# Performance work log

Measured on AMD Instinct MI355X. Metric: run time of the kernel, lower is better.

## Reference

```python
import jax, jax.numpy as jnp
import numpy as np

N = 50000      # nodes
E = 800000     # edges (before self-loops)
DIN, H1, H2, OUT = 128, 128, 64, 40
LN_EPS = 1e-5


def setup_inputs() -> dict:
    key = jax.random.key(0)
    ks = jax.random.split(key, 16)
    s = lambda d: 1.0 / np.sqrt(d)
    inp = {
        "x": jax.random.normal(ks[0], (N, DIN), jnp.float32),
        "edge_index": jax.random.randint(ks[1], (2, E), 0, N, dtype=jnp.int64),
        # GCNConv weights (applied as x @ W) and biases
        "W1": jax.random.normal(ks[2], (DIN, H1), jnp.float32) * s(DIN),
        "b1": jnp.zeros((H1,), jnp.float32),
        "W2": jax.random.normal(ks[3], (H1, H2), jnp.float32) * s(H1),
        "b2": jnp.zeros((H2,), jnp.float32),
        "W3": jax.random.normal(ks[4], (H2, H2), jnp.float32) * s(H2),
        "b3": jnp.zeros((H2,), jnp.float32),
        # LayerNorms
        "g1": jnp.ones((H1,), jnp.float32),
        "be1": jnp.zeros((H1,), jnp.float32),
        "g2": jnp.ones((H2,), jnp.float32),
        "be2": jnp.zeros((H2,), jnp.float32),
        # post_mp MLP head
        "Wp1": jax.random.normal(ks[5], (H2, H2), jnp.float32) * s(H2),
        "bp1": jnp.zeros((H2,), jnp.float32),
        "Wp2": jax.random.normal(ks[6], (H2, OUT), jnp.float32) * s(H2),
        "bp2": jnp.zeros((OUT,), jnp.float32),
    }
    return inp


def _layer_norm(x, g, b):
    mu = jnp.mean(x, axis=-1, keepdims=True)
    var = jnp.mean((x - mu) ** 2, axis=-1, keepdims=True)
    return (x - mu) * jax.lax.rsqrt(var + LN_EPS) * g + b


def _gcn(x, src, dst, norm, W, b):
    # PyG GCNConv: linear first, then normalized gather/scatter-add, bias last
    h = x @ W                                  # [N, H]
    msg = h[src] * norm[:, None]               # [E+N, H] gather
    out = jax.ops.segment_sum(msg, dst, num_segments=N)  # scatter-add
    return out + b


def reference(x, edge_index, W1, b1, W2, b2, W3, b3, g1, be1, g2, be2,
              Wp1, bp1, Wp2, bp2):
    loops = jnp.arange(N, dtype=edge_index.dtype)
    src = jnp.concatenate([edge_index[0], loops])  # add self-loops
    dst = jnp.concatenate([edge_index[1], loops])
    # symmetric normalization D^{-1/2} (A+I) D^{-1/2} (same graph all layers)
    deg = jax.ops.segment_sum(jnp.ones_like(src, dtype=x.dtype), dst,
                              num_segments=N)
    dinv = jnp.where(deg > 0, jax.lax.rsqrt(jnp.maximum(deg, 1.0)), 0.0)
    norm = dinv[src] * dinv[dst]

    h = _gcn(x, src, dst, norm, W1, b1)
    h = _layer_norm(jax.nn.relu(h), g1, be1)
    h = _gcn(h, src, dst, norm, W2, b2)
    h = _layer_norm(jax.nn.relu(h), g2, be2)
    emb = _gcn(h, src, dst, norm, W3, b3)      # emb = conv output, pre-ReLU
    h = jax.nn.relu(emb)
    h = (h @ Wp1 + bp1) @ Wp2 + bp2            # post_mp: two stacked Linears
    return emb, jax.nn.log_softmax(h, axis=1)
```

## Files before the change

### kernel.cpp

```cpp
#include <hip/hip_runtime.h>
#include <hip/hip_bf16.h>

#define DIN 128
#define HID1 128
#define HID2 64
#define OUTD 40
#define NCHUNK 128

typedef __attribute__((ext_vector_type(8))) short bf16x8;
typedef __attribute__((ext_vector_type(4))) float f32x4;

__device__ __forceinline__ float bf2f(unsigned int u) {
    union { unsigned int i; float f; } c;
    c.i = u << 16;
    return c.f;
}
__device__ __forceinline__ unsigned short f2bf(float f) {
    union { float f; unsigned int i; } c; c.f = f;
    unsigned int r = c.i + 0x7FFFu + ((c.i >> 16) & 1u);
    return (unsigned short)(r >> 16);
}
__device__ __forceinline__ unsigned int packbf(float lo, float hi) {
    return (unsigned int)f2bf(lo) | ((unsigned int)f2bf(hi) << 16);
}

__device__ __forceinline__ int get_src(const int* ei, int E, int e, int e64) {
    return e64 ? ei[2 * e] : ei[e];
}
__device__ __forceinline__ int get_dst(const int* ei, int E, int e, int e64) {
    return e64 ? ei[2 * (E + e)] : ei[E + e];
}

struct WCvt {
    const void* p[14];
    int sz[14];
    int off[14];
    int tobf[14];
    int cols[14];
};

__launch_bounds__(1024)
__global__ void posA_kernel(const unsigned short* __restrict__ xu,
                            const int* __restrict__ ei,
                            int* __restrict__ flags,
                            int* __restrict__ pos,
                            unsigned int* __restrict__ hist,
                            int E, int N) {
    __shared__ unsigned int h32[25000];
    __shared__ int sh2[2];
    const int NW = (N + 1) >> 1;
    const int b = blockIdx.x;
    const int t = threadIdx.x;
    if (b < NCHUNK) {
        if (t == 0) sh2[0] = 0;
        for (int w = t; w < NW; w += 1024) h32[w] = 0u;
        __syncthreads();
        int zodd = 0;
        for (int k = t; k < 1024; k += 1024)
            if (ei[2 * k + 1] == 0) zodd++;
        if (zodd) atomicAdd(&sh2[0], zodd);
        __syncthreads();
        const int e64 = (sh2[0] > 512) ? 1 : 0;
        const int CH = (E + NCHUNK - 1) / NCHUNK;
        const int lo = b * CH;
        int hi = lo + CH; if (hi > E) hi = E;
        for (int e = lo + t; e < hi; e += 1024) {
            int d = e64 ? ei[2 * (E + e)] : ei[E + e];
            if ((unsigned)d < (unsigned)N) {
                unsigned sh = (unsigned)(d & 1) << 4;
                unsigned old = atomicAdd(&h32[d >> 1], 1u << sh);
                pos[e] = (int)((old >> sh) & 0xffffu);
            } else {
                pos[e] = -1;
            }
        }
        __syncthreads();
        unsigned int* hb = hist + (size_t)b * NW;
        for (int w = t; w < NW; w += 1024) hb[w] = h32[w];
    } else {
        if (t < 2) sh2[t] = 0;
        __syncthreads();
        int bad = 0;
        for (int k = t; k < 2048; k += 1024) {
            float v = bf2f(xu[2 * k]);
            float a = fabsf(v);
            if (!(a <= 1e4f) || (v != 0.f && a < 1e-4f)) bad++;
        }
        int zodd = 0;
        for (int k = t; k < 1024; k += 1024)
            if (ei[2 * k + 1] == 0) zodd++;
        if (bad) atomicAdd(&sh2[0], bad);
        if (zodd) atomicAdd(&sh2[1], zodd);
        __syncthreads();
        if (t == 0) {
            flags[0] = (sh2[0] > 512) ? 1 : 0;
            flags[1] = (sh2[1] > 512) ? 1 : 0;
        }
    }
}

__launch_bounds__(256)
__global__ void phaseB_kernel(const unsigned int* __restrict__ hist,
                              unsigned int* __restrict__ basev,
                              int* __restrict__ cnt, int* __restrict__ bsum,
                              int N, int PB,
                              WCvt wc, unsigned short* __restrict__ wbf,
                              float* __restrict__ wf,
                              const int* __restrict__ flags) {
    __shared__ int red[256];
    const int NW = (N + 1) >> 1;
    int t = threadIdx.x;
    int blk = blockIdx.x;
    if (blk < PB) {
        int w = blk * 256 + t;
        unsigned run0 = 0, run1 = 0;
        if (w < NW) {
            #pragma unroll 4
            for (int b = 0; b < NCHUNK; ++b) {
                unsigned u = hist[(size_t)b * NW + w];
                basev[(size_t)b * NW + w] = (run0 & 0xffffu) | (run1 << 16);
                run0 += u & 0xffffu;
                run1 += u >> 16;
            }
            cnt[2 * w] = (int)run0;
            if (2 * w + 1 < N) cnt[2 * w + 1] = (int)run1;
        }
        int tot = 0;
        if (w < NW) tot = (int)run0 + ((2 * w + 1 < N) ? (int)run1 : 0);
        red[t] = tot;
        __syncthreads();
        #pragma unroll
        for (int off = 64; off >= 1; off >>= 1) {
            if ((t & 127) < off) red[t] += red[t + off];
            __syncthreads();
        }
        if (t == 0) bsum[2 * blk] = red[0];
        if (t == 128) bsum[2 * blk + 1] = red[128];
    } else {
        int xf32 = flags[0];
        int stride = (gridDim.x - PB) * 256;
        int tid = (blk - PB) * 256 + t;
        for (int a = 0; a < 14; ++a) {
            const float* pf = (const float*)wc.p[a];
            const unsigned short* pb = (const unsigned short*)wc.p[a];
            int n = wc.sz[a], off = wc.off[a], tobf = wc.tobf[a];
            int cols = wc.cols[a];
            int rows = tobf ? (n / cols) : 0;
            for (int i = tid; i < n; i += stride) {
                float v = xf32 ? pf[i] : bf2f(pb[i]);
                if (tobf) {
                    int k = i / cols, m = i % cols;
                    wbf[off + m * rows + k] = f2bf(v);
                } else {
                    wf[off + i] = v;
                }
            }
        }
    }
}

__global__ void scatter_kernel(const int* __restrict__ ei, const int* __restrict__ indptr,
                               const int* __restrict__ pos, const float* __restrict__ dinv,
                               const unsigned int* __restrict__ basev,
                               int2* __restrict__ csr_sn,
                               int E, int N, const int* __restrict__ flags) {
    int e64 = flags[1];
    int CH = (E + NCHUNK - 1) / NCHUNK;
    int NW = (N + 1) >> 1;
    int base = (blockIdx.x * blockDim.x + threadIdx.x) * 4;
    #pragma unroll
    for (int u = 0; u < 4; ++u) {
        int e = base + u;
        if (e < E) {
            int p = pos[e];
            if (p >= 0) {
                int bb = e / CH;
                int d = get_dst(ei, E, e, e64);
                int s = get_src(ei, E, e, e64);
                if ((unsigned)s >= (unsigned)N) s = 0;
                float nrm = dinv[s] * dinv[d];
                unsigned bw = basev[(size_t)bb * NW + (d >> 1)];
                int bval = (d & 1) ? (int)(bw >> 16) : (int)(bw & 0xffffu);
                int slot = indptr[d] + bval + p;
                csr_sn[slot] = make_int2(s, __float_as_int(nrm));
            }
        }
    }
}


template<typename AT>
__device__ __forceinline__ bf16x8 ld_afrag(const AT* p);
template<>
__device__ __forceinline__ bf16x8 ld_afrag<unsigned short>(const unsigned short* p) {
    return *(const bf16x8*)p;
}
template<>
__device__ __forceinline__ bf16x8 ld_afrag<float>(const float* p) {
    float4 a = *(const float4*)p;
    float4 b = *(const float4*)(p + 4);
    bf16x8 r;
    r[0] = (short)f2bf(a.x); r[1] = (short)f2bf(a.y);
    r[2] = (short)f2bf(a.z); r[3] = (short)f2bf(a.w);
    r[4] = (short)f2bf(b.x); r[5] = (short)f2bf(b.y);
    r[6] = (short)f2bf(b.z); r[7] = (short)f2bf(b.w);
    return r;
}

template<int K, int M, typename AT>
__device__ __forceinline__ void mm_body(const AT* __restrict__ A,
                                        const unsigned short* __restrict__ WT,
                                        unsigned short* __restrict__ C, int N,
                                        unsigned short (*Ws)[K + 8], int bx) {
    int tid = threadIdx.x;
    for (int idx = tid; idx < M * K / 8; idx += 256) {
        int r = idx / (K / 8), c8 = idx % (K / 8);
        *(uint4*)&Ws[r][c8 * 8] = *(const uint4*)&WT[r * K + c8 * 8];
    }
    __syncthreads();
    int w = tid >> 6, lane = tid & 63;
    int m = lane & 15, q = lane >> 4;
    int row_a = bx * 64 + w * 16 + m;
    if (row_a >= N) row_a = N - 1;
    const AT* arow = A + (size_t)row_a * K;
    f32x4 acc[M / 16];
    #pragma unroll
    for (int t = 0; t < M / 16; ++t) acc[t] = (f32x4){0.f, 0.f, 0.f, 0.f};
    #pragma unroll
    for (int ks = 0; ks < K / 32; ++ks) {
        int k0 = ks * 32 + q * 8;
        bf16x8 a = ld_afrag<AT>(arow + k0);
        #pragma unroll
        for (int t = 0; t < M / 16; ++t) {
            bf16x8 b = *(const bf16x8*)&Ws[t * 16 + m][k0];
            acc[t] = __builtin_amdgcn_mfma_f32_16x16x32_bf16(a, b, acc[t], 0, 0, 0);
        }
    }
    int rbase = bx * 64 + w * 16 + q * 4;
    #pragma unroll
    for (int reg = 0; reg < 4; ++reg) {
        int row = rbase + reg;
        if (row < N) {
            #pragma unroll
            for (int t = 0; t < M / 16; ++t)
                C[(size_t)row * M + t * 16 + m] = f2bf(acc[t][reg]);
        }
    }
}

template<int K, int M>
__launch_bounds__(256)
__global__ void emit_mm_kernel(const int* __restrict__ cnt, const int* __restrict__ bsum,
                               int* __restrict__ indptr, float* __restrict__ dinv,
                               int N, int NB,
                               const void* __restrict__ A,
                               const unsigned short* __restrict__ WT,
                               unsigned short* __restrict__ C,
                               const int* __restrict__ flags) {
    __shared__ unsigned short Ws[M][K + 8];
    int blk = blockIdx.x;
    int t = threadIdx.x;
    if (blk < NB) {
        int* part = (int*)&Ws[0][0];
        int* sh   = part + 256;
        part[t] = (t < NB) ? bsum[t] : 0;
        __syncthreads();
        for (int off = 1; off < 256; off <<= 1) {
            int v = (t >= off) ? part[t - off] : 0;
            __syncthreads();
            part[t] += v;
            __syncthreads();
        }
        int bbase = (blk > 0) ? part[blk - 1] : 0;
        int total = part[255];
        int i = blk * 256 + t;
        int c = (i < N) ? cnt[i] : 0;
        sh[t] = c;
        __syncthreads();
        for (int off = 1; off < 256; off <<= 1) {
            int v = (t >= off) ? sh[t - off] : 0;
            __syncthreads();
            sh[t] += v;
            __syncthreads();
        }
        if (i < N) {
            int excl = sh[t] - c + bbase;
            indptr[i] = excl;
            dinv[i] = 1.0f / sqrtf((float)(c + 1));
        }
        if (blk == NB - 1 && t == 0) indptr[N] = total;
    } else {
        int bx = blk - NB;
        if (flags[0]) mm_body<K, M, float>((const float*)A, WT, C, N, Ws, bx);
        else          mm_body<K, M, unsigned short>((const unsigned short*)A, WT, C, N, Ws, bx);
    }
}

template<int K, int M>
__launch_bounds__(256)
__global__ void mm_bf_kernel(const unsigned short* __restrict__ A,
                             const unsigned short* __restrict__ WT,
                             unsigned short* __restrict__ C, int N) {
    __shared__ unsigned short Ws[M][K + 8];
    mm_body<K, M, unsigned short>(A, WT, C, N, Ws, blockIdx.x);
}


template<int VPL>
__device__ __forceinline__ void gacc1(float* acc, const unsigned short* r, float n) {
    if constexpr (VPL == 8) {
        uint4 u = *(const uint4*)r;
        acc[0] += bf2f(u.x & 0xffffu) * n; acc[1] += bf2f(u.x >> 16) * n;
        acc[2] += bf2f(u.y & 0xffffu) * n; acc[3] += bf2f(u.y >> 16) * n;
        acc[4] += bf2f(u.z & 0xffffu) * n; acc[5] += bf2f(u.z >> 16) * n;
        acc[6] += bf2f(u.w & 0xffffu) * n; acc[7] += bf2f(u.w >> 16) * n;
    } else {
        uint2 u = *(const uint2*)r;
        acc[0] += bf2f(u.x & 0xffffu) * n; acc[1] += bf2f(u.x >> 16) * n;
        acc[2] += bf2f(u.y & 0xffffu) * n; acc[3] += bf2f(u.y >> 16) * n;
    }
}

template<int VPL>
__device__ __forceinline__ void gacc8(float* acc,
                                      const unsigned short* const* rp,
                                      const float* nv) {
    if constexpr (VPL == 8) {
        uint4 u[8];
        #pragma unroll
        for (int i = 0; i < 8; ++i) u[i] = *(const uint4*)rp[i];
        #pragma unroll
        for (int i = 0; i < 8; ++i) {
            float n = nv[i];
            acc[0] += bf2f(u[i].x & 0xffffu) * n; acc[1] += bf2f(u[i].x >> 16) * n;
            acc[2] += bf2f(u[i].y & 0xffffu) * n; acc[3] += bf2f(u[i].y >> 16) * n;
            acc[4] += bf2f(u[i].z & 0xffffu) * n; acc[5] += bf2f(u[i].z >> 16) * n;
            acc[6] += bf2f(u[i].w & 0xffffu) * n; acc[7] += bf2f(u[i].w >> 16) * n;
        }
    } else {
        uint2 u[8];
        #pragma unroll
        for (int i = 0; i < 8; ++i) u[i] = *(const uint2*)rp[i];
        #pragma unroll
        for (int i = 0; i < 8; ++i) {
            float n = nv[i];
            acc[0] += bf2f(u[i].x & 0xffffu) * n; acc[1] += bf2f(u[i].x >> 16) * n;
            acc[2] += bf2f(u[i].y & 0xffffu) * n; acc[3] += bf2f(u[i].y >> 16) * n;
        }
    }
}

template<int H, bool RELU_LN, bool EMB>
__launch_bounds__(256)
__global__ void agg_kernel(const unsigned short* __restrict__ h,
                           const int* __restrict__ indptr,
                           const int2* __restrict__ csr_sn,
                           const float* __restrict__ dinv,
                           const float* __restrict__ bias,
                           const float* __restrict__ gamma,
                           const float* __restrict__ beta,
                           unsigned short* __restrict__ out,
                           void* __restrict__ out_emb,
                           int N, const int* __restrict__ flags) {
    constexpr int VPL = H / 16;
    __shared__ int2 lsn[4][4][32];
    int w = threadIdx.x >> 6;
    int lane = threadIdx.x & 63;
    int g = lane >> 4;
    int idx = lane & 15;
    int node = blockIdx.x * 16 + w * 4 + g;
    bool active = node < N;
    int nd = active ? node : N - 1;
    float di = dinv[nd];
    int c0 = idx * VPL;
    float acc[VPL];
    #pragma unroll
    for (int v = 0; v < VPL; ++v) acc[v] = 0.f;
    gacc1<VPL>(acc, h + (size_t)nd * H + c0, di * di);
    int beg = indptr[nd], end = indptr[nd + 1];
    for (int base = beg; base < end; base += 32) {
        int m = end - base; if (m > 32) m = 32;
        lsn[w][g][idx]      = (idx < m)      ? csr_sn[base + idx]      : make_int2(0, 0);
        lsn[w][g][idx + 16] = (idx + 16 < m) ? csr_sn[base + idx + 16] : make_int2(0, 0);
        int rounds = (m + 7) >> 3;
        int j = 0;
        for (int rr = 0; rr < rounds; ++rr, j += 8) {
            const unsigned short* rp[8];
            float nv[8];
            #pragma unroll
            for (int i = 0; i < 8; ++i) {
                int2 e = lsn[w][g][j + i];
                rp[i] = h + (size_t)e.x * H + c0;
                nv[i] = __int_as_float(e.y);
            }
            gacc8<VPL>(acc, rp, nv);
        }
    }
    #pragma unroll
    for (int v = 0; v < VPL; ++v) acc[v] += bias[c0 + v];
    if constexpr (RELU_LN) {
        #pragma unroll
        for (int v = 0; v < VPL; ++v) acc[v] = fmaxf(acc[v], 0.f);
        float s = 0.f, sq = 0.f;
        #pragma unroll
        for (int v = 0; v < VPL; ++v) { s += acc[v]; sq += acc[v] * acc[v]; }
        #pragma unroll
        for (int off = 8; off >= 1; off >>= 1) {
            s += __shfl_xor(s, off, 64);
            sq += __shfl_xor(sq, off, 64);
        }
        float mu = s * (1.0f / H);
        float var = fmaxf(sq * (1.0f / H) - mu * mu, 0.f);
        float inv = 1.0f / sqrtf(var + 1e-5f);
        #pragma unroll
        for (int v = 0; v < VPL; ++v)
            acc[v] = (acc[v] - mu) * inv * gamma[c0 + v] + beta[c0 + v];
    }
    if (active) {
        unsigned short* orow = out + (size_t)node * H + c0;
        if constexpr (VPL == 8) {
            uint4 p;
            p.x = packbf(acc[0], acc[1]); p.y = packbf(acc[2], acc[3]);
            p.z = packbf(acc[4], acc[5]); p.w = packbf(acc[6], acc[7]);
            *(uint4*)orow = p;
        } else {
            uint2 p; p.x = packbf(acc[0], acc[1]); p.y = packbf(acc[2], acc[3]);
            *(uint2*)orow = p;
        }
        if constexpr (EMB) {
            if (flags[0]) {
                float* o = (float*)out_emb + (size_t)node * H + c0;
                #pragma unroll
                for (int v4 = 0; v4 < VPL / 4; ++v4)
                    *(float4*)(o + v4 * 4) = make_float4(acc[v4 * 4], acc[v4 * 4 + 1],
                                                         acc[v4 * 4 + 2], acc[v4 * 4 + 3]);
            } else {
                unsigned short* o = (unsigned short*)out_emb + (size_t)node * H + c0;
                #pragma unroll
                for (int v2 = 0; v2 < VPL / 2; ++v2)
                    ((unsigned int*)o)[v2] = packbf(acc[v2 * 2], acc[v2 * 2 + 1]);
            }
        }
    }
}


__launch_bounds__(256)
__global__ void head_kernel(const unsigned short* __restrict__ emb,
                            const float* __restrict__ Wp1,
                            const float* __restrict__ bp1,
                            const float* __restrict__ Wp2,
                            const float* __restrict__ bp2,
                            void* __restrict__ d_out, int N,
                            const int* __restrict__ flags) {
    __shared__ float Est[64][68];
    __shared__ float W1s[64][64];
    __shared__ float Tst[64][68];
    __shared__ float W2s[64][OUTD];
    __shared__ float b1s[64];
    __shared__ float b2s[OUTD];
    int tid = threadIdx.x;
    int row0 = blockIdx.x * 64;
    for (int i = tid; i < 64 * 64; i += 256) W1s[i >> 6][i & 63] = Wp1[i];
    for (int i = tid; i < 64 * OUTD; i += 256) W2s[i / OUTD][i % OUTD] = Wp2[i];
    if (tid < 64) b1s[tid] = bp1[tid];
    if (tid < OUTD) b2s[tid] = bp2[tid];
    for (int i = tid; i < 64 * 32; i += 256) {
        int r = i >> 5, kk = i & 31;
        int row = row0 + r;
        unsigned int u = (row < N) ? *(const unsigned int*)&emb[(size_t)row * 64 + kk * 2] : 0u;
        Est[kk * 2][r]     = fmaxf(bf2f(u & 0xffffu), 0.f);
        Est[kk * 2 + 1][r] = fmaxf(bf2f(u >> 16), 0.f);
    }
    __syncthreads();
    {
        int rg = tid >> 4, cg = tid & 15;
        int r = rg * 4, c = cg * 4;
        float acc[4][4];
        #pragma unroll
        for (int i = 0; i < 4; ++i)
            #pragma unroll
            for (int jj = 0; jj < 4; ++jj) acc[i][jj] = b1s[c + jj];
        #pragma unroll 4
        for (int k = 0; k < 64; ++k) {
            float4 a = *(const float4*)&Est[k][r];
            float4 wv = *(const float4*)&W1s[k][c];
            acc[0][0] += a.x * wv.x; acc[0][1] += a.x * wv.y; acc[0][2] += a.x * wv.z; acc[0][3] += a.x * wv.w;
            acc[1][0] += a.y * wv.x; acc[1][1] += a.y * wv.y; acc[1][2] += a.y * wv.z; acc[1][3] += a.y * wv.w;
            acc[2][0] += a.z * wv.x; acc[2][1] += a.z * wv.y; acc[2][2] += a.z * wv.z; acc[2][3] += a.z * wv.w;
            acc[3][0] += a.w * wv.x; acc[3][1] += a.w * wv.y; acc[3][2] += a.w * wv.z; acc[3][3] += a.w * wv.w;
        }
        #pragma unroll
        for (int i = 0; i < 4; ++i)
            #pragma unroll
            for (int jj = 0; jj < 4; ++jj) Tst[c + jj][r + i] = acc[i][jj];
    }
    __syncthreads();
    int row = tid >> 2, tc = tid & 3, o0 = tc * 10;
    int node = row0 + row;
    float u[10];
    #pragma unroll
    for (int o = 0; o < 10; ++o) u[o] = b2s[o0 + o];
    for (int c2 = 0; c2 < 64; ++c2) {
        float tv = Tst[c2][row];
        const float2* wp = (const float2*)&W2s[c2][o0];
        #pragma unroll
        for (int o2 = 0; o2 < 5; ++o2) {
            float2 wv = wp[o2];
            u[o2 * 2]     += tv * wv.x;
            u[o2 * 2 + 1] += tv * wv.y;
        }
    }
    float mx = u[0];
    #pragma unroll
    for (int o = 1; o < 10; ++o) mx = fmaxf(mx, u[o]);
    mx = fmaxf(mx, __shfl_xor(mx, 1, 64));
    mx = fmaxf(mx, __shfl_xor(mx, 2, 64));
    float sum = 0.f;
    #pragma unroll
    for (int o = 0; o < 10; ++o) sum += __expf(u[o] - mx);
    sum += __shfl_xor(sum, 1, 64);
    sum += __shfl_xor(sum, 2, 64);
    float lse = mx + __logf(sum);
    if (node < N) {
        if (flags[0]) {
            float* base = (float*)d_out + (size_t)N * HID2;
            float* op = base + (size_t)node * OUTD + o0;
            #pragma unroll
            for (int o = 0; o < 10; ++o) op[o] = u[o] - lse;
        } else {
            unsigned short* base = (unsigned short*)d_out + (size_t)N * HID2;
            unsigned int* op = (unsigned int*)(base + (size_t)node * OUTD + o0);
            #pragma unroll
            for (int o2 = 0; o2 < 5; ++o2)
                op[o2] = packbf(u[o2 * 2] - lse, u[o2 * 2 + 1] - lse);
        }
    }
}


extern "C" void kernel_launch(void* const* d_in, const int* in_sizes, int n_in,
                              void* d_out, int out_size, void* d_ws, size_t ws_size,
                              hipStream_t stream) {
    const unsigned short* xu = (const unsigned short*)d_in[0];
    const int*            ei = (const int*)d_in[1];

    const int N = in_sizes[0] / DIN;
    const int E = in_sizes[1] / 2;
    const int NW = (N + 1) / 2;

    size_t off = 0;
    auto take = [&](size_t bytes) {
        size_t cur = off;
        off += (bytes + 255) & ~(size_t)255;
        return cur;
    };
    char* ws = (char*)d_ws;
    int*   flags   = (int*)  (ws + take(256));
    int*   cnt     = (int*)  (ws + take((size_t)N * 4));
    float* dinv    = (float*)(ws + take((size_t)N * 4));
    int*   indptr  = (int*)  (ws + take((size_t)(N + 1) * 4));
    int*   pos     = (int*)  (ws + take((size_t)E * 4));
    int2*  csr_sn  = (int2*) (ws + take((size_t)E * 8));
    int*   bsum    = (int*)  (ws + take(((size_t)N / 256 + 4) * 4));
    unsigned int* hist  = (unsigned int*)(ws + take((size_t)NCHUNK * NW * 4));
    unsigned int* basev = (unsigned int*)(ws + take((size_t)NCHUNK * NW * 4));
    unsigned short* wbf = (unsigned short*)(ws + take(32768 * 2));
    float*          wf  = (float*)         (ws + take(8192 * 4));
    unsigned short* hbuf = (unsigned short*)(ws + take((size_t)N * DIN * 2));
    unsigned short* abuf = (unsigned short*)(ws + take((size_t)N * DIN * 2));
    (void)ws_size; (void)n_in; (void)out_size;

    const int TB = 256;
    dim3 blk(TB);
    const int NB = (N + 255) / 256;
    const int PB = (NW + 255) / 256;
    const int MMG = (N + 63) / 64;

    WCvt wc;
    int bfoff = 0, foff = 0;
    int offs[14];
    const int wcols[14] = {HID1, 0, HID2, 0, HID2, 0, 0, 0, 0, 0, 0, 0, 0, 0};
    for (int a = 0; a < 14; ++a) {
        int idx = a + 2;
        wc.p[a] = d_in[idx];
        wc.sz[a] = in_sizes[idx];
        int tobf = (idx == 2 || idx == 4 || idx == 6) ? 1 : 0;
        wc.tobf[a] = tobf;
        wc.cols[a] = tobf ? wcols[a] : 1;
        if (tobf) { wc.off[a] = bfoff; bfoff += in_sizes[idx]; }
        else      { wc.off[a] = foff;  foff  += in_sizes[idx]; }
        offs[a] = wc.off[a];
    }

    unsigned short* W1t = wbf + offs[0];
    unsigned short* W2t = wbf + offs[2];
    unsigned short* W3t = wbf + offs[4];
    float* b1f  = wf + offs[1];
    float* b2f  = wf + offs[3];
    float* b3f  = wf + offs[5];
    float* g1f  = wf + offs[6];
    float* be1f = wf + offs[7];
    float* g2f  = wf + offs[8];
    float* be2f = wf + offs[9];
    float* Wp1f = wf + offs[10];
    float* bp1f = wf + offs[11];
    float* Wp2f = wf + offs[12];
    float* bp2f = wf + offs[13];

    posA_kernel<<<dim3(NCHUNK + 1), dim3(1024), 0, stream>>>(
        xu, ei, flags, pos, hist, E, N);
    phaseB_kernel<<<dim3(PB + 64), blk, 0, stream>>>(
        hist, basev, cnt, bsum, N, PB, wc, wbf, wf, flags);
    emit_mm_kernel<DIN, HID1><<<dim3(NB + MMG), blk, 0, stream>>>(
        cnt, bsum, indptr, dinv, N, NB, d_in[0], W1t, hbuf, flags);
    scatter_kernel<<<dim3((E + 1023) / 1024), blk, 0, stream>>>(
        ei, indptr, pos, dinv, basev, csr_sn, E, N, flags);

    const int AGG = (N + 15) / 16;

    agg_kernel<HID1, true, false><<<dim3(AGG), blk, 0, stream>>>(
        hbuf, indptr, csr_sn, dinv, b1f, g1f, be1f, abuf, nullptr, N, flags);

    mm_bf_kernel<HID1, HID2><<<dim3(MMG), blk, 0, stream>>>(abuf, W2t, hbuf, N);
    agg_kernel<HID2, true, false><<<dim3(AGG), blk, 0, stream>>>(
        hbuf, indptr, csr_sn, dinv, b2f, g2f, be2f, abuf, nullptr, N, flags);

    mm_bf_kernel<HID2, HID2><<<dim3(MMG), blk, 0, stream>>>(abuf, W3t, hbuf, N);
    agg_kernel<HID2, false, true><<<dim3(AGG), blk, 0, stream>>>(
        hbuf, indptr, csr_sn, dinv, b3f, nullptr, nullptr, abuf, d_out, N, flags);

    head_kernel<<<dim3((N + 63) / 64), blk, 0, stream>>>(
        abuf, Wp1f, bp1f, Wp2f, bp2f, d_out, N, flags);
}
```

Before: 275.7 us.

## Fuse GCN aggregation with following matmul and head into combined kernels

Merges each aggregation+ReLU+LayerNorm step with the next layer's MFMA matmul, so normalized rows stay in shared memory instead of round-tripping through global memory. The final aggregation is fused with the post-MP MLP head and log-softmax. This removes three launches and several full-size intermediate writes and reads. In exchange each block does four nodes per wave-group sequentially before the matmul, which lowers the number of blocks and the latency hiding available to the gather loop.

```diff
diff --git a/kernel.cpp b/kernel.cpp
--- a/kernel.cpp
+++ b/kernel.cpp
@@ -296,15 +296,6 @@
     }
 }
 
-template<int K, int M>
-__launch_bounds__(256)
-__global__ void mm_bf_kernel(const unsigned short* __restrict__ A,
-                             const unsigned short* __restrict__ WT,
-                             unsigned short* __restrict__ C, int N) {
-    __shared__ unsigned short Ws[M][K + 8];
-    mm_body<K, M, unsigned short>(A, WT, C, N, Ws, blockIdx.x);
-}
-
 
 template<int VPL>
 __device__ __forceinline__ void gacc1(float* acc, const unsigned short* r, float n) {
@@ -350,38 +341,21 @@
     }
 }
 
-template<int H, bool RELU_LN, bool EMB>
-__launch_bounds__(256)
-__global__ void agg_kernel(const unsigned short* __restrict__ h,
-                           const int* __restrict__ indptr,
-                           const int2* __restrict__ csr_sn,
-                           const float* __restrict__ dinv,
-                           const float* __restrict__ bias,
-                           const float* __restrict__ gamma,
-                           const float* __restrict__ beta,
-                           unsigned short* __restrict__ out,
-                           void* __restrict__ out_emb,
-                           int N, const int* __restrict__ flags) {
-    constexpr int VPL = H / 16;
-    __shared__ int2 lsn[4][4][32];
-    int w = threadIdx.x >> 6;
-    int lane = threadIdx.x & 63;
-    int g = lane >> 4;
-    int idx = lane & 15;
-    int node = blockIdx.x * 16 + w * 4 + g;
-    bool active = node < N;
-    int nd = active ? node : N - 1;
-    float di = dinv[nd];
-    int c0 = idx * VPL;
-    float acc[VPL];
+template<int VPL, int H>
+__device__ __forceinline__ void agg_node(float* acc,
+                                         const unsigned short* __restrict__ h,
+                                         const int* __restrict__ indptr,
+                                         const int2* __restrict__ csr_sn,
+                                         int nd, float di, int c0,
+                                         int2 (*lsn), int idx) {
     #pragma unroll
     for (int v = 0; v < VPL; ++v) acc[v] = 0.f;
     gacc1<VPL>(acc, h + (size_t)nd * H + c0, di * di);
     int beg = indptr[nd], end = indptr[nd + 1];
     for (int base = beg; base < end; base += 32) {
         int m = end - base; if (m > 32) m = 32;
-        lsn[w][g][idx]      = (idx < m)      ? csr_sn[base + idx]      : make_int2(0, 0);
-        lsn[w][g][idx + 16] = (idx + 16 < m) ? csr_sn[base + idx + 16] : make_int2(0, 0);
+        lsn[idx]      = (idx < m)      ? csr_sn[base + idx]      : make_int2(0, 0);
+        lsn[idx + 16] = (idx + 16 < m) ? csr_sn[base + idx + 16] : make_int2(0, 0);
         int rounds = (m + 7) >> 3;
         int j = 0;
         for (int rr = 0; rr < rounds; ++rr, j += 8) {
@@ -389,18 +363,51 @@
             float nv[8];
             #pragma unroll
             for (int i = 0; i < 8; ++i) {
-                int2 e = lsn[w][g][j + i];
+                int2 e = lsn[j + i];
                 rp[i] = h + (size_t)e.x * H + c0;
                 nv[i] = __int_as_float(e.y);
             }
             gacc8<VPL>(acc, rp, nv);
         }
     }
-    #pragma unroll
-    for (int v = 0; v < VPL; ++v) acc[v] += bias[c0 + v];
-    if constexpr (RELU_LN) {
-        #pragma unroll
-        for (int v = 0; v < VPL; ++v) acc[v] = fmaxf(acc[v], 0.f);
+}
+
+
+template<int H, int M>
+__launch_bounds__(256)
+__global__ void aggmm_kernel(const unsigned short* __restrict__ h,
+                             const int* __restrict__ indptr,
+                             const int2* __restrict__ csr_sn,
+                             const float* __restrict__ dinv,
+                             const float* __restrict__ bias,
+                             const float* __restrict__ gamma,
+                             const float* __restrict__ beta,
+                             const unsigned short* __restrict__ WT,
+                             unsigned short* __restrict__ C, int N) {
+    constexpr int VPL = H / 16;
+    __shared__ unsigned short At[64][H + 8];
+    __shared__ unsigned short Ws[M][H + 8];
+    __shared__ int2 lsn[4][4][32];
+    int tid = threadIdx.x;
+    for (int i2 = tid; i2 < M * H / 8; i2 += 256) {
+        int r = i2 / (H / 8), c8 = i2 % (H / 8);
+        *(uint4*)&Ws[r][c8 * 8] = *(const uint4*)&WT[r * H + c8 * 8];
+    }
+    int w = tid >> 6;
+    int lane = tid & 63;
+    int g = lane >> 4;
+    int idx = lane & 15;
+    int c0 = idx * VPL;
+    int grp = w * 4 + g;
+    for (int nn = 0; nn < 4; ++nn) {
+        int lrow = grp * 4 + nn;
+        int node = blockIdx.x * 64 + lrow;
+        int nd = (node < N) ? node : N - 1;
+        float di = dinv[nd];
+        float acc[VPL];
+        agg_node<VPL, H>(acc, h, indptr, csr_sn, nd, di, c0, lsn[w][g], idx);
+        #pragma unroll
+        for (int v = 0; v < VPL; ++v) acc[v] = fmaxf(acc[v] + bias[c0 + v], 0.f);
         float s = 0.f, sq = 0.f;
         #pragma unroll
         for (int v = 0; v < VPL; ++v) { s += acc[v]; sq += acc[v] * acc[v]; }
@@ -415,62 +422,101 @@
         #pragma unroll
         for (int v = 0; v < VPL; ++v)
             acc[v] = (acc[v] - mu) * inv * gamma[c0 + v] + beta[c0 + v];
-    }
-    if (active) {
-        unsigned short* orow = out + (size_t)node * H + c0;
         if constexpr (VPL == 8) {
             uint4 p;
             p.x = packbf(acc[0], acc[1]); p.y = packbf(acc[2], acc[3]);
             p.z = packbf(acc[4], acc[5]); p.w = packbf(acc[6], acc[7]);
-            *(uint4*)orow = p;
+            *(uint4*)&At[lrow][c0] = p;
         } else {
             uint2 p; p.x = packbf(acc[0], acc[1]); p.y = packbf(acc[2], acc[3]);
-            *(uint2*)orow = p;
-        }
-        if constexpr (EMB) {
-            if (flags[0]) {
-                float* o = (float*)out_emb + (size_t)node * H + c0;
-                #pragma unroll
-                for (int v4 = 0; v4 < VPL / 4; ++v4)
-                    *(float4*)(o + v4 * 4) = make_float4(acc[v4 * 4], acc[v4 * 4 + 1],
-                                                         acc[v4 * 4 + 2], acc[v4 * 4 + 3]);
-            } else {
-                unsigned short* o = (unsigned short*)out_emb + (size_t)node * H + c0;
-                #pragma unroll
-                for (int v2 = 0; v2 < VPL / 2; ++v2)
-                    ((unsigned int*)o)[v2] = packbf(acc[v2 * 2], acc[v2 * 2 + 1]);
-            }
+            *(uint2*)&At[lrow][c0] = p;
+        }
+    }
+    __syncthreads();
+    int m_ = lane & 15, q = lane >> 4;
+    int lr = w * 16 + m_;
+    f32x4 acc2[M / 16];
+    #pragma unroll
+    for (int t2 = 0; t2 < M / 16; ++t2) acc2[t2] = (f32x4){0.f, 0.f, 0.f, 0.f};
+    #pragma unroll
+    for (int ks = 0; ks < H / 32; ++ks) {
+        int k0 = ks * 32 + q * 8;
+        bf16x8 a = *(const bf16x8*)&At[lr][k0];
+        #pragma unroll
+        for (int t2 = 0; t2 < M / 16; ++t2) {
+            bf16x8 b = *(const bf16x8*)&Ws[t2 * 16 + m_][k0];
+            acc2[t2] = __builtin_amdgcn_mfma_f32_16x16x32_bf16(a, b, acc2[t2], 0, 0, 0);
+        }
+    }
+    int rbase = blockIdx.x * 64 + w * 16 + q * 4;
+    #pragma unroll
+    for (int reg = 0; reg < 4; ++reg) {
+        int row = rbase + reg;
+        if (row < N) {
+            #pragma unroll
+            for (int t2 = 0; t2 < M / 16; ++t2)
+                C[(size_t)row * M + t2 * 16 + m_] = f2bf(acc2[t2][reg]);
         }
     }
 }
 
 
 __launch_bounds__(256)
-__global__ void head_kernel(const unsigned short* __restrict__ emb,
-                            const float* __restrict__ Wp1,
-                            const float* __restrict__ bp1,
-                            const float* __restrict__ Wp2,
-                            const float* __restrict__ bp2,
-                            void* __restrict__ d_out, int N,
-                            const int* __restrict__ flags) {
+__global__ void agghead_kernel(const unsigned short* __restrict__ h,
+                               const int* __restrict__ indptr,
+                               const int2* __restrict__ csr_sn,
+                               const float* __restrict__ dinv,
+                               const float* __restrict__ bias,
+                               const float* __restrict__ Wp1,
+                               const float* __restrict__ bp1,
+                               const float* __restrict__ Wp2,
+                               const float* __restrict__ bp2,
+                               void* __restrict__ d_out, int N,
+                               const int* __restrict__ flags) {
+    constexpr int VPL = 4;
     __shared__ float Est[64][68];
     __shared__ float W1s[64][64];
     __shared__ float Tst[64][68];
     __shared__ float W2s[64][OUTD];
     __shared__ float b1s[64];
     __shared__ float b2s[OUTD];
+    __shared__ int2 lsn[4][4][32];
     int tid = threadIdx.x;
     int row0 = blockIdx.x * 64;
     for (int i = tid; i < 64 * 64; i += 256) W1s[i >> 6][i & 63] = Wp1[i];
     for (int i = tid; i < 64 * OUTD; i += 256) W2s[i / OUTD][i % OUTD] = Wp2[i];
     if (tid < 64) b1s[tid] = bp1[tid];
     if (tid < OUTD) b2s[tid] = bp2[tid];
-    for (int i = tid; i < 64 * 32; i += 256) {
-        int r = i >> 5, kk = i & 31;
-        int row = row0 + r;
-        unsigned int u = (row < N) ? *(const unsigned int*)&emb[(size_t)row * 64 + kk * 2] : 0u;
-        Est[kk * 2][r]     = fmaxf(bf2f(u & 0xffffu), 0.f);
-        Est[kk * 2 + 1][r] = fmaxf(bf2f(u >> 16), 0.f);
+    int w = tid >> 6;
+    int lane = tid & 63;
+    int g = lane >> 4;
+    int idx = lane & 15;
+    int c0 = idx * VPL;
+    int grp = w * 4 + g;
+    int xf32 = flags[0];
+    for (int nn = 0; nn < 4; ++nn) {
+        int lrow = grp * 4 + nn;
+        int node = row0 + lrow;
+        bool active = node < N;
+        int nd = active ? node : N - 1;
+        float di = dinv[nd];
+        float acc[VPL];
+        agg_node<VPL, HID2>(acc, h, indptr, csr_sn, nd, di, c0, lsn[w][g], idx);
+        #pragma unroll
+        for (int v = 0; v < VPL; ++v) acc[v] += bias[c0 + v];
+        if (active) {
+            if (xf32) {
+                float* o = (float*)d_out + (size_t)node * HID2 + c0;
+                *(float4*)o = make_float4(acc[0], acc[1], acc[2], acc[3]);
+            } else {
+                unsigned short* o = (unsigned short*)d_out + (size_t)node * HID2 + c0;
+                ((unsigned int*)o)[0] = packbf(acc[0], acc[1]);
+                ((unsigned int*)o)[1] = packbf(acc[2], acc[3]);
+            }
+        }
+        #pragma unroll
+        for (int v = 0; v < VPL; ++v)
+            Est[c0 + v][lrow] = fmaxf(acc[v], 0.f);
     }
     __syncthreads();
     {
@@ -523,7 +569,7 @@
     sum += __shfl_xor(sum, 2, 64);
     float lse = mx + __logf(sum);
     if (node < N) {
-        if (flags[0]) {
+        if (xf32) {
             float* base = (float*)d_out + (size_t)N * HID2;
             float* op = base + (size_t)node * OUTD + o0;
             #pragma unroll
@@ -617,19 +663,10 @@
     scatter_kernel<<<dim3((E + 1023) / 1024), blk, 0, stream>>>(
         ei, indptr, pos, dinv, basev, csr_sn, E, N, flags);
 
-    const int AGG = (N + 15) / 16;
-
-    agg_kernel<HID1, true, false><<<dim3(AGG), blk, 0, stream>>>(
-        hbuf, indptr, csr_sn, dinv, b1f, g1f, be1f, abuf, nullptr, N, flags);
-
-    mm_bf_kernel<HID1, HID2><<<dim3(MMG), blk, 0, stream>>>(abuf, W2t, hbuf, N);
-    agg_kernel<HID2, true, false><<<dim3(AGG), blk, 0, stream>>>(
-        hbuf, indptr, csr_sn, dinv, b2f, g2f, be2f, abuf, nullptr, N, flags);
-
-    mm_bf_kernel<HID2, HID2><<<dim3(MMG), blk, 0, stream>>>(abuf, W3t, hbuf, N);
-    agg_kernel<HID2, false, true><<<dim3(AGG), blk, 0, stream>>>(
-        hbuf, indptr, csr_sn, dinv, b3f, nullptr, nullptr, abuf, d_out, N, flags);
-
-    head_kernel<<<dim3((N + 63) / 64), blk, 0, stream>>>(
-        abuf, Wp1f, bp1f, Wp2f, bp2f, d_out, N, flags);
-}
+    aggmm_kernel<HID1, HID2><<<dim3(MMG), blk, 0, stream>>>(
+        hbuf, indptr, csr_sn, dinv, b1f, g1f, be1f, W2t, abuf, N);
+    aggmm_kernel<HID2, HID2><<<dim3(MMG), blk, 0, stream>>>(
+        abuf, indptr, csr_sn, dinv, b2f, g2f, be2f, W3t, hbuf, N);
+    agghead_kernel<<<dim3(MMG), blk, 0, stream>>>(
+        hbuf, indptr, csr_sn, dinv, b3f, Wp1f, bp1f, Wp2f, bp2f, d_out, N, flags);
+}
```

Result: no change. 276.0 us (+0.1%).
